# Kernel optimization log

Hardware: AMD Instinct MI355X
Metric: run time of the kernel (lower is better)

The kernel has to match this reference:

```python
import jax, jax.numpy as jnp
import numpy as np

N = 50000
E = 800000
NUM_GRAPHS = 128
X_IN, HID, EDGE_DIM = 64, 64, 16


def setup_inputs() -> dict:
    key = jax.random.key(0)
    ks = jax.random.split(key, 9)
    s = 0.05
    inp = {
        'x': jax.random.normal(ks[0], (N, X_IN), jnp.float32),
        'edge_index': jax.random.randint(ks[1], (2, E), 0, N, dtype=jnp.int32),
        'edge_attr': jax.random.normal(ks[2], (E, EDGE_DIM), jnp.float32),
        'batch': jnp.sort(jax.random.randint(ks[3], (N,), 0, NUM_GRAPHS, dtype=jnp.int32)),
        'w_fc1': jax.random.normal(ks[4], (EDGE_DIM, 1), jnp.float32) * s,
        'b_fc1': jnp.zeros((1,), jnp.float32),
    }
    dims = [(X_IN, HID), (HID, HID * 2), (HID * 2, HID)]
    for i, (din, dout) in enumerate(dims):
        k1, k2, k3 = jax.random.split(ks[5 + i], 3)
        inp[f'w1_{i}'] = jax.random.normal(k1, (din, dout), jnp.float32) * s
        inp[f'b1_{i}'] = jnp.zeros((dout,), jnp.float32)
        inp[f'w2_{i}'] = jax.random.normal(k2, (din, dout), jnp.float32) * s
        inp[f'w3_{i}'] = jax.random.normal(k3, (din, dout), jnp.float32) * s
        inp[f'b3_{i}'] = jnp.zeros((dout,), jnp.float32)
    return inp


def leconv(x, src, dst, ew, w1, b1, w2, w3, b3):
    # PyG LEConv: out_i = lin3(x_i) + sum_{j->i} e_ji * (lin1(x_j) - lin2(x_i))
    a = x @ w1 + b1          # lin1 (bias=True)   [N, out]
    b = x @ w2               # lin2 (bias=False)  [N, out]
    msg = ew[:, None] * (a[src] - b[dst])          # [E, out]
    agg = jax.ops.segment_sum(msg, dst, num_segments=N)
    return agg + x @ w3 + b3  # lin3 (bias=True)


def reference(x, edge_index, edge_attr, batch,
              w_fc1, b_fc1,
              w1_0, b1_0, w2_0, w3_0, b3_0,
              w1_1, b1_1, w2_1, w3_1, b3_1,
              w1_2, b1_2, w2_2, w3_2, b3_2):
    src, dst = edge_index[0], edge_index[1]
    ew = (edge_attr @ w_fc1 + b_fc1)[:, 0]         # fc1(edge_attr).squeeze(-1) -> [E]
    h = jax.nn.elu(leconv(x, src, dst, ew, w1_0, b1_0, w2_0, w3_0, b3_0))
    h = jax.nn.elu(leconv(h, src, dst, ew, w1_1, b1_1, w2_1, w3_1, b3_1))
    h = jax.nn.elu(leconv(h, src, dst, ew, w1_2, b1_2, w2_2, w3_2, b3_2))
    # global max pool over nodes of each graph -> [NUM_GRAPHS, HID]
    return jax.ops.segment_max(h, batch, num_segments=NUM_GRAPHS)
```

## Files before the change

kernel.cpp:

```cpp
#include <hip/hip_runtime.h>
#include <math.h>

#define N_NODES 50000
#define N_EDGES 800000
#define NUM_GRAPHS_ 128
#define SCAN_NB 98
#define NPASS 8
#define NODES_PER_PASS 6250
#define HCHUNKS 128
#define EDGES_PER_CHUNK 6250
#define HWORDS 12500

typedef unsigned short u16;
typedef unsigned int u32;
typedef __attribute__((ext_vector_type(8))) short bf16x8;
typedef __attribute__((ext_vector_type(4))) float f32x4;

__device__ __forceinline__ float elu_f(float v) {
    return v > 0.f ? v : (__expf(v) - 1.f);
}
__device__ __forceinline__ u16 f2bf(float f) {
    u32 u = __float_as_uint(f);
    u += 0x7FFFu + ((u >> 16) & 1u);
    return (u16)(u >> 16);
}
__device__ __forceinline__ float bf2f(u16 h) {
    return __uint_as_float(((u32)h) << 16);
}
__device__ __forceinline__ void bfpair(u32 v, float& lo, float& hi) {
    lo = __uint_as_float(v << 16);
    hi = __uint_as_float(v & 0xFFFF0000u);
}
__device__ __forceinline__ u32 packbf(float lo, float hi) {
    return (u32)f2bf(lo) | ((u32)f2bf(hi) << 16);
}

__global__ void conv_x_kernel(const float* __restrict__ x, u16* __restrict__ xb) {
    int g = blockIdx.x * blockDim.x + threadIdx.x;
    float4 v = ((const float4*)x)[g];
    uint2 o;
    o.x = packbf(v.x, v.y);
    o.y = packbf(v.z, v.w);
    ((uint2*)xb)[g] = o;
}

__global__ void ew_kernel(const float* __restrict__ edge_attr,
                          const float* __restrict__ w_fc1,
                          const float* __restrict__ b_fc1,
                          const int* __restrict__ edge_index,
                          float* __restrict__ ew,
                          u16* __restrict__ dst16) {
    int e = blockIdx.x * blockDim.x + threadIdx.x;
    if (e >= N_EDGES) return;
    const float4* ea = (const float4*)(edge_attr + (size_t)e * 16);
    const float4* wf = (const float4*)w_fc1;
    float acc = b_fc1[0];
#pragma unroll
    for (int i = 0; i < 4; i++) {
        float4 a = ea[i], w = wf[i];
        acc += a.x * w.x + a.y * w.y + a.z * w.z + a.w * w.w;
    }
    ew[e] = acc;
    dst16[e] = (u16)edge_index[N_EDGES + e];
}

__global__ __launch_bounds__(256) void deg_hist_kernel(const u16* __restrict__ dst16,
                                                       u32* __restrict__ partial) {
    __shared__ u32 bins[HWORDS];
    const int c = blockIdx.x >> 1;
    const int p = blockIdx.x & 1;
    const int t = threadIdx.x;
    for (int i = t; i < HWORDS; i += 256) bins[i] = 0;
    __syncthreads();
    const int base = c * EDGES_PER_CHUNK;
    const int nlo = p * 25000;
    for (int i = t; i < EDGES_PER_CHUNK; i += 256) {
        const int b = (int)dst16[base + i] - nlo;
        if ((unsigned)b < 25000u)
            atomicAdd(&bins[b >> 1], 1u << ((b & 1) * 16));
    }
    __syncthreads();
    u32* outp = partial + (size_t)blockIdx.x * HWORDS;
    for (int i = t; i < HWORDS; i += 256) outp[i] = bins[i];
}

__global__ void deg_reduce_kernel(const u32* __restrict__ partial,
                                  u32* __restrict__ deg4) {
    const int tidg = blockIdx.x * 256 + threadIdx.x;
    if (tidg >= 25000) return;
    const int p = (tidg >= HWORDS) ? 1 : 0;
    const int w = tidg - p * HWORDS;
    const int y = blockIdx.y;
    u32 lo = 0, hi = 0;
#pragma unroll 8
    for (int j = 0; j < 32; j++) {
        u32 v = partial[(size_t)(((y * 32 + j) << 1) + p) * HWORDS + w];
        lo += v & 0xFFFFu;
        hi += v >> 16;
    }
    const int n = p * 25000 + 2 * w;
    deg4[(size_t)y * N_NODES + n] = lo;
    deg4[(size_t)y * N_NODES + n + 1] = hi;
}

__global__ __launch_bounds__(256) void scan1_kernel(const u32* __restrict__ deg4,
                                                    int* __restrict__ rowptr,
                                                    int* __restrict__ blk_sums) {
    __shared__ int sh[256];
    const int t = threadIdx.x;
    const int base = blockIdx.x * 512;
    const int i0 = base + 2 * t, i1 = i0 + 1;
    int d0 = 0, d1 = 0;
    if (i0 < N_NODES) {
#pragma unroll
        for (int y = 0; y < 4; y++) {
            d0 += (int)deg4[(size_t)y * N_NODES + i0];
            d1 += (int)deg4[(size_t)y * N_NODES + i1];
        }
    }
    const int pair = d0 + d1;
    int v = pair;
    sh[t] = v;
    __syncthreads();
#pragma unroll
    for (int off = 1; off < 256; off <<= 1) {
        int add = (t >= off) ? sh[t - off] : 0;
        __syncthreads();
        v += add;
        sh[t] = v;
        __syncthreads();
    }
    const int excl = v - pair;
    if (i0 < N_NODES) rowptr[i0] = excl;
    if (i1 < N_NODES) rowptr[i1] = excl + d0;
    if (t == 255) blk_sums[blockIdx.x] = v;
}

__global__ __launch_bounds__(128) void scan2_kernel(const int* __restrict__ blk_sums,
                                                    int* __restrict__ blk_offs,
                                                    int* __restrict__ rowptr) {
    __shared__ int sh[128];
    const int t = threadIdx.x;
    const int orig = (t < SCAN_NB) ? blk_sums[t] : 0;
    int v = orig;
    sh[t] = v;
    __syncthreads();
#pragma unroll
    for (int off = 1; off < 128; off <<= 1) {
        int add = (t >= off) ? sh[t - off] : 0;
        __syncthreads();
        v += add;
        sh[t] = v;
        __syncthreads();
    }
    if (t < SCAN_NB) blk_offs[t] = v - orig;
    if (t == 127) rowptr[N_NODES] = v;
}

__global__ void scan3_kernel(int* __restrict__ rowptr,
                             const int* __restrict__ blk_offs,
                             int* __restrict__ cursor) {
    int i = blockIdx.x * blockDim.x + threadIdx.x;
    if (i >= N_NODES) return;
    int r = rowptr[i] + blk_offs[i >> 9];
    rowptr[i] = r;
    cursor[i] = r;
}

__global__ __launch_bounds__(256) void place_kernel(const int* __restrict__ edge_index,
                                                    const float* __restrict__ ew,
                                                    const u16* __restrict__ dst16,
                                                    int* __restrict__ cursor,
                                                    int2* __restrict__ csr) {
    const int pass = blockIdx.x & (NPASS - 1);
    const int chunk = blockIdx.x >> 3;
    const int lo = pass * NODES_PER_PASS;
    const int hi = lo + NODES_PER_PASS;
    const int base = chunk * 1024 + threadIdx.x;
#pragma unroll
    for (int u = 0; u < 4; u++) {
        const int e = base + u * 256;
        if (e >= N_EDGES) break;
        const int d = (int)dst16[e];
        if (d >= lo && d < hi) {
            int pos = atomicAdd(&cursor[d], 1);
            int2 ent;
            ent.x = edge_index[e];
            ent.y = __float_as_int(ew[e]);
            csr[pos] = ent;
        }
    }
}

template <int DIN, bool WRITE_C>
__global__ __launch_bounds__(256) void gather_kernel(
    const u16* __restrict__ xb, const int* __restrict__ rowptr,
    const int2* __restrict__ csr, u16* __restrict__ sb,
    u16* __restrict__ chb, float* __restrict__ c) {
    constexpr int CG = DIN / 4;
    constexpr int EG = 64 / CG;
    const int gid = blockIdx.x * 256 + threadIdx.x;
    const int node = gid >> 6;
    if (node >= N_NODES) return;
    const int lane = threadIdx.x & 63;
    const int cg = lane & (CG - 1);
    const int eg = lane / CG;
    const int beg = rowptr[node];
    const int end = rowptr[node + 1];
    const uint2* x2 = (const uint2*)xb;

    float a0 = 0.f, a1 = 0.f, a2 = 0.f, a3 = 0.f;
    float b0 = 0.f, b1 = 0.f, b2 = 0.f, b3 = 0.f;
    float wsum = 0.f;

    int p = beg + eg;
    for (; p + EG < end; p += 2 * EG) {
        int2 e0 = csr[p];
        int2 e1 = csr[p + EG];
        float w0 = __int_as_float(e0.y);
        float w1 = __int_as_float(e1.y);
        uint2 v0 = x2[(size_t)e0.x * CG + cg];
        uint2 v1 = x2[(size_t)e1.x * CG + cg];
        float f0, f1, f2, f3, g0, g1, g2, g3;
        bfpair(v0.x, f0, f1); bfpair(v0.y, f2, f3);
        bfpair(v1.x, g0, g1); bfpair(v1.y, g2, g3);
        a0 += w0 * f0; a1 += w0 * f1; a2 += w0 * f2; a3 += w0 * f3;
        b0 += w1 * g0; b1 += w1 * g1; b2 += w1 * g2; b3 += w1 * g3;
        wsum += w0 + w1;
    }
    if (p < end) {
        int2 e0 = csr[p];
        float w0 = __int_as_float(e0.y);
        uint2 v0 = x2[(size_t)e0.x * CG + cg];
        float f0, f1, f2, f3;
        bfpair(v0.x, f0, f1); bfpair(v0.y, f2, f3);
        a0 += w0 * f0; a1 += w0 * f1; a2 += w0 * f2; a3 += w0 * f3;
        wsum += w0;
    }
    a0 += b0; a1 += b1; a2 += b2; a3 += b3;

#pragma unroll
    for (int off = 32; off >= CG; off >>= 1) {
        a0 += __shfl_xor(a0, off);
        a1 += __shfl_xor(a1, off);
        a2 += __shfl_xor(a2, off);
        a3 += __shfl_xor(a3, off);
        wsum += __shfl_xor(wsum, off);
    }

    if (lane < CG) {
        uint2 so;
        so.x = packbf(a0, a1);
        so.y = packbf(a2, a3);
        ((uint2*)sb)[(size_t)node * CG + cg] = so;
        const float cn = WRITE_C ? wsum : c[node];
        uint2 hv = x2[(size_t)node * CG + cg];
        float h0, h1, h2, h3;
        bfpair(hv.x, h0, h1); bfpair(hv.y, h2, h3);
        uint2 co;
        co.x = packbf(cn * h0, cn * h1);
        co.y = packbf(cn * h2, cn * h3);
        ((uint2*)chb)[(size_t)node * CG + cg] = co;
    }
    if (WRITE_C && lane == 0) c[node] = wsum;
}

__global__ void pack_w_kernel(const float* __restrict__ w3_0, const float* __restrict__ w1_0, const float* __restrict__ w2_0,
                              const float* __restrict__ w3_1, const float* __restrict__ w1_1, const float* __restrict__ w2_1,
                              const float* __restrict__ w3_2, const float* __restrict__ w1_2, const float* __restrict__ w2_2,
                              u16* __restrict__ bp0, u16* __restrict__ bp1, u16* __restrict__ bp2) {
    int t = blockIdx.x * blockDim.x + threadIdx.x;
    if (t >= 7680) return;
    int DIN, DOUT, lid;
    const float *w3, *w1, *w2;
    u16* bp;
    if (t < 1536)      { DIN = 64;  DOUT = 64;  lid = t;        w3 = w3_0; w1 = w1_0; w2 = w2_0; bp = bp0; }
    else if (t < 4608) { DIN = 64;  DOUT = 128; lid = t - 1536; w3 = w3_1; w1 = w1_1; w2 = w2_1; bp = bp1; }
    else               { DIN = 128; DOUT = 64;  lid = t - 4608; w3 = w3_2; w1 = w1_2; w2 = w2_2; bp = bp2; }
    const int NT = DOUT / 16;
    const int lane = lid & 63;
    const int fragid = lid >> 6;
    const int chunk = fragid / NT;
    const int ntile = fragid % NT;
    const int n = ntile * 16 + (lane & 15);
    const int kbase = chunk * 32 + (lane >> 4) * 8;
    u16 buf[8];
#pragma unroll
    for (int j = 0; j < 8; j++) {
        int k = kbase + j;
        int region = k / DIN;
        int kk = k - region * DIN;
        float v = (region == 0) ? w3[kk * DOUT + n]
                : (region == 1) ? w1[kk * DOUT + n]
                                : -w2[kk * DOUT + n];
        buf[j] = f2bf(v);
    }
    *(bf16x8*)(bp + ((size_t)lid << 3)) = *(bf16x8*)buf;
}

template <int DIN, int DOUT>
__global__ __launch_bounds__(256) void gemm_mfma(
    const u16* __restrict__ hb, const u16* __restrict__ sb,
    const u16* __restrict__ chb, const u16* __restrict__ Bp,
    const float* __restrict__ cvec, const float* __restrict__ bias1,
    const float* __restrict__ bias3, u16* __restrict__ outp) {
    constexpr int CH = DIN / 32;
    constexpr int CHUNKS = 3 * CH;
    constexpr int NT = DOUT / 16;
    const int tid = threadIdx.x;
    const int wv = tid >> 6;
    const int lane = tid & 63;
    const int l15 = lane & 15;
    const int q = lane >> 4;
    const int mhalf = wv & 1;
    const int nhalf = wv >> 1;
    const int row_base = blockIdx.x * 64 + mhalf * 32;
    const int nt0 = blockIdx.y * 4 + nhalf * 2;

    const int r0 = min(row_base + l15, N_NODES - 1);
    const int r1 = min(row_base + 16 + l15, N_NODES - 1);
    const int qo = q * 8;

    f32x4 acc00 = {0.f, 0.f, 0.f, 0.f};
    f32x4 acc01 = {0.f, 0.f, 0.f, 0.f};
    f32x4 acc10 = {0.f, 0.f, 0.f, 0.f};
    f32x4 acc11 = {0.f, 0.f, 0.f, 0.f};

#pragma unroll
    for (int chunk = 0; chunk < CHUNKS; chunk++) {
        const int region = chunk / CH;
        const int koff = (chunk - region * CH) * 32 + qo;
        const u16* A = (region == 0) ? hb : (region == 1) ? sb : chb;
        bf16x8 a0 = *(const bf16x8*)(A + (size_t)r0 * DIN + koff);
        bf16x8 a1 = *(const bf16x8*)(A + (size_t)r1 * DIN + koff);
        const u16* bp = Bp + (((size_t)(chunk * NT + nt0) * 64 + lane) << 3);
        bf16x8 bf0 = *(const bf16x8*)bp;
        bf16x8 bf1 = *(const bf16x8*)(bp + 64 * 8);
        acc00 = __builtin_amdgcn_mfma_f32_16x16x32_bf16(a0, bf0, acc00, 0, 0, 0);
        acc01 = __builtin_amdgcn_mfma_f32_16x16x32_bf16(a0, bf1, acc01, 0, 0, 0);
        acc10 = __builtin_amdgcn_mfma_f32_16x16x32_bf16(a1, bf0, acc10, 0, 0, 0);
        acc11 = __builtin_amdgcn_mfma_f32_16x16x32_bf16(a1, bf1, acc11, 0, 0, 0);
    }

#pragma unroll
    for (int ni = 0; ni < 2; ni++) {
        const int col = (nt0 + ni) * 16 + l15;
        const float B3 = bias3[col];
        const float B1 = bias1[col];
        const f32x4 am0 = ni ? acc01 : acc00;
        const f32x4 am1 = ni ? acc11 : acc10;
#pragma unroll
        for (int mi = 0; mi < 2; mi++) {
            const f32x4 av = mi ? am1 : am0;
#pragma unroll
            for (int reg = 0; reg < 4; reg++) {
                const int row = row_base + mi * 16 + q * 4 + reg;
                if (row < N_NODES) {
                    const float cv = cvec[row];
                    const float val = av[reg] + B3 + cv * B1;
                    outp[(size_t)row * DOUT + col] = f2bf(elu_f(val));
                }
            }
        }
    }
}

__global__ void pool_kernel(const u16* __restrict__ h,
                            const int* __restrict__ batch,
                            float* __restrict__ out) {
    const int g = blockIdx.x;
    const int tid = threadIdx.x;
    int lo = 0, hi = N_NODES;
    while (lo < hi) { int mid = (lo + hi) >> 1; if (batch[mid] < g) lo = mid + 1; else hi = mid; }
    const int beg = lo;
    lo = beg; hi = N_NODES;
    while (lo < hi) { int mid = (lo + hi) >> 1; if (batch[mid] < g + 1) lo = mid + 1; else hi = mid; }
    const int end = lo;

    __shared__ float red[256];
    const int col = tid & 63;
    const int rg = tid >> 6;
    float m = -3.0e38f;
    for (int r = beg + rg; r < end; r += 4) m = fmaxf(m, bf2f(h[(size_t)r * 64 + col]));
    red[tid] = m;
    __syncthreads();
    if (tid < 64) {
        m = fmaxf(fmaxf(red[tid], red[tid + 64]), fmaxf(red[tid + 128], red[tid + 192]));
        out[g * 64 + tid] = m;
    }
}

extern "C" void kernel_launch(void* const* d_in, const int* in_sizes, int n_in,
                              void* d_out, int out_size, void* d_ws, size_t ws_size,
                              hipStream_t stream) {
    const float* x = (const float*)d_in[0];
    const int* ei = (const int*)d_in[1];
    const float* ea = (const float*)d_in[2];
    const int* batch = (const int*)d_in[3];
    const float* wfc = (const float*)d_in[4];
    const float* bfc = (const float*)d_in[5];
    const float* w1_0 = (const float*)d_in[6];
    const float* b1_0 = (const float*)d_in[7];
    const float* w2_0 = (const float*)d_in[8];
    const float* w3_0 = (const float*)d_in[9];
    const float* b3_0 = (const float*)d_in[10];
    const float* w1_1 = (const float*)d_in[11];
    const float* b1_1 = (const float*)d_in[12];
    const float* w2_1 = (const float*)d_in[13];
    const float* w3_1 = (const float*)d_in[14];
    const float* b3_1 = (const float*)d_in[15];
    const float* w1_2 = (const float*)d_in[16];
    const float* b1_2 = (const float*)d_in[17];
    const float* w2_2 = (const float*)d_in[18];
    const float* w3_2 = (const float*)d_in[19];
    const float* b3_2 = (const float*)d_in[20];
    float* out = (float*)d_out;

    char* ws = (char*)d_ws;
    float* ew      = (float*)(ws);
    float* c       = (float*)(ws + 3200000);
    int*   cursor  = (int*)  (ws + 3600000);
    int*   rowptr  = (int*)  (ws + 3800000);
    int2*  csr     = (int2*) (ws + 4000128);
    u16*   xb      = (u16*)  (ws + 10400128);
    u16*   sb      = (u16*)  (ws + 16800128);
    u16*   chb     = (u16*)  (ws + 29600128);
    u16*   h1      = (u16*)  (ws + 42400128);
    u16*   h2      = (u16*)  (ws + 48800128);
    u16*   h3      = (u16*)  (ws + 61600128);
    u16*   bp0     = (u16*)  (ws + 68000128);
    u16*   bp1     = (u16*)  (ws + 68024704);
    u16*   bp2     = (u16*)  (ws + 68073856);
    int* blk_sums  = (int*)  (ws + 68123008);
    int* blk_offs  = (int*)  (ws + 68123520);
    u16* dst16   = chb;
    u32* deg4    = (u32*)(ws + 31600128);
    u32* partial = (u32*)sb;

    conv_x_kernel<<<3125, 256, 0, stream>>>(x, xb);
    ew_kernel<<<(N_EDGES + 255) / 256, 256, 0, stream>>>(ea, wfc, bfc, ei, ew, dst16);
    pack_w_kernel<<<30, 256, 0, stream>>>(w3_0, w1_0, w2_0, w3_1, w1_1, w2_1,
                                          w3_2, w1_2, w2_2, bp0, bp1, bp2);
    deg_hist_kernel<<<HCHUNKS * 2, 256, 0, stream>>>(dst16, partial);
    deg_reduce_kernel<<<dim3(98, 4), 256, 0, stream>>>(partial, deg4);
    scan1_kernel<<<SCAN_NB, 256, 0, stream>>>(deg4, rowptr, blk_sums);
    scan2_kernel<<<1, 128, 0, stream>>>(blk_sums, blk_offs, rowptr);
    scan3_kernel<<<(N_NODES + 255) / 256, 256, 0, stream>>>(rowptr, blk_offs, cursor);
    place_kernel<<<782 * NPASS, 256, 0, stream>>>(ei, ew, dst16, cursor, csr);

    const int RB = (N_NODES + 63) / 64;
    const int GBLK = (N_NODES * 64 + 255) / 256;

    gather_kernel<64, true><<<GBLK, 256, 0, stream>>>(xb, rowptr, csr, sb, chb, c);
    gemm_mfma<64, 64><<<dim3(RB, 1), 256, 0, stream>>>(xb, sb, chb, bp0, c, b1_0, b3_0, h1);

    gather_kernel<64, false><<<GBLK, 256, 0, stream>>>(h1, rowptr, csr, sb, chb, c);
    gemm_mfma<64, 128><<<dim3(RB, 2), 256, 0, stream>>>(h1, sb, chb, bp1, c, b1_1, b3_1, h2);

    gather_kernel<128, false><<<GBLK, 256, 0, stream>>>(h2, rowptr, csr, sb, chb, c);
    gemm_mfma<128, 64><<<dim3(RB, 1), 256, 0, stream>>>(h2, sb, chb, bp2, c, b1_2, b3_2, h3);

    pool_kernel<<<NUM_GRAPHS_, 256, 0, stream>>>(h3, batch, out);
}
```

Before: 369.8 us.

## Make CSR placement deterministic and reorder last layer to transform-then-gather

```diff
diff --git a/kernel.cpp b/kernel.cpp
--- a/kernel.cpp
+++ b/kernel.cpp
@@ -84,26 +84,24 @@
     for (int i = t; i < HWORDS; i += 256) outp[i] = bins[i];
 }
 
-__global__ void deg_reduce_kernel(const u32* __restrict__ partial,
-                                  u32* __restrict__ deg4) {
-    const int tidg = blockIdx.x * 256 + threadIdx.x;
-    if (tidg >= 25000) return;
-    const int p = (tidg >= HWORDS) ? 1 : 0;
-    const int w = tidg - p * HWORDS;
-    const int y = blockIdx.y;
-    u32 lo = 0, hi = 0;
-#pragma unroll 8
-    for (int j = 0; j < 32; j++) {
-        u32 v = partial[(size_t)(((y * 32 + j) << 1) + p) * HWORDS + w];
-        lo += v & 0xFFFFu;
-        hi += v >> 16;
-    }
-    const int n = p * 25000 + 2 * w;
-    deg4[(size_t)y * N_NODES + n] = lo;
-    deg4[(size_t)y * N_NODES + n + 1] = hi;
-}
-
-__global__ __launch_bounds__(256) void scan1_kernel(const u32* __restrict__ deg4,
+__global__ __launch_bounds__(256) void scan_chunks_kernel(const u32* __restrict__ partial,
+                                                          u32* __restrict__ prefpack,
+                                                          u32* __restrict__ degpack) {
+    const int g = blockIdx.x * 256 + threadIdx.x;
+    if (g >= 25000) return;
+    const int p = (g >= HWORDS) ? 1 : 0;
+    const int wh = g - p * HWORDS;
+    u32 runlo = 0, runhi = 0;
+    for (int c = 0; c < HCHUNKS; c++) {
+        prefpack[(size_t)c * 25000 + g] = runlo | (runhi << 16);
+        u32 v = partial[(size_t)((c << 1) + p) * HWORDS + wh];
+        runlo += v & 0xFFFFu;
+        runhi += v >> 16;
+    }
+    degpack[g] = runlo | (runhi << 16);
+}
+
+__global__ __launch_bounds__(256) void scan1_kernel(const u32* __restrict__ degpack,
                                                     int* __restrict__ rowptr,
                                                     int* __restrict__ blk_sums) {
     __shared__ int sh[256];
@@ -112,11 +110,9 @@
     const int i0 = base + 2 * t, i1 = i0 + 1;
     int d0 = 0, d1 = 0;
     if (i0 < N_NODES) {
-#pragma unroll
-        for (int y = 0; y < 4; y++) {
-            d0 += (int)deg4[(size_t)y * N_NODES + i0];
-            d1 += (int)deg4[(size_t)y * N_NODES + i1];
-        }
+        u32 v = degpack[i0 >> 1];
+        d0 = (int)(v & 0xFFFFu);
+        d1 = (int)(v >> 16);
     }
     const int pair = d0 + d1;
     int v = pair;
@@ -158,36 +154,38 @@
 }
 
 __global__ void scan3_kernel(int* __restrict__ rowptr,
-                             const int* __restrict__ blk_offs,
-                             int* __restrict__ cursor) {
+                             const int* __restrict__ blk_offs) {
     int i = blockIdx.x * blockDim.x + threadIdx.x;
     if (i >= N_NODES) return;
-    int r = rowptr[i] + blk_offs[i >> 9];
-    rowptr[i] = r;
-    cursor[i] = r;
+    rowptr[i] += blk_offs[i >> 9];
 }
 
 __global__ __launch_bounds__(256) void place_kernel(const int* __restrict__ edge_index,
                                                     const float* __restrict__ ew,
                                                     const u16* __restrict__ dst16,
-                                                    int* __restrict__ cursor,
+                                                    const int* __restrict__ rowptr,
+                                                    const u32* __restrict__ prefpack,
                                                     int2* __restrict__ csr) {
+    __shared__ int lcur[NODES_PER_PASS];
     const int pass = blockIdx.x & (NPASS - 1);
-    const int chunk = blockIdx.x >> 3;
+    const int c = blockIdx.x >> 3;
     const int lo = pass * NODES_PER_PASS;
-    const int hi = lo + NODES_PER_PASS;
-    const int base = chunk * 1024 + threadIdx.x;
-#pragma unroll
-    for (int u = 0; u < 4; u++) {
-        const int e = base + u * 256;
-        if (e >= N_EDGES) break;
+    const int t = threadIdx.x;
+    for (int i = t; i < NODES_PER_PASS; i += 256) lcur[i] = 0;
+    __syncthreads();
+    const int base = c * EDGES_PER_CHUNK;
+    for (int i = t; i < EDGES_PER_CHUNK; i += 256) {
+        const int e = base + i;
         const int d = (int)dst16[e];
-        if (d >= lo && d < hi) {
-            int pos = atomicAdd(&cursor[d], 1);
+        const int dl = d - lo;
+        if ((unsigned)dl < (unsigned)NODES_PER_PASS) {
+            u32 pw = prefpack[(size_t)c * 25000 + (d >> 1)];
+            int pref = (int)((pw >> ((d & 1) * 16)) & 0xFFFFu);
+            int lpos = atomicAdd(&lcur[dl], 1);
             int2 ent;
             ent.x = edge_index[e];
             ent.y = __float_as_int(ew[e]);
-            csr[pos] = ent;
+            csr[rowptr[d] + pref + lpos] = ent;
         }
     }
 }
@@ -271,31 +269,50 @@
                               u16* __restrict__ bp0, u16* __restrict__ bp1, u16* __restrict__ bp2) {
     int t = blockIdx.x * blockDim.x + threadIdx.x;
     if (t >= 7680) return;
-    int DIN, DOUT, lid;
-    const float *w3, *w1, *w2;
-    u16* bp;
-    if (t < 1536)      { DIN = 64;  DOUT = 64;  lid = t;        w3 = w3_0; w1 = w1_0; w2 = w2_0; bp = bp0; }
-    else if (t < 4608) { DIN = 64;  DOUT = 128; lid = t - 1536; w3 = w3_1; w1 = w1_1; w2 = w2_1; bp = bp1; }
-    else               { DIN = 128; DOUT = 64;  lid = t - 4608; w3 = w3_2; w1 = w1_2; w2 = w2_2; bp = bp2; }
-    const int NT = DOUT / 16;
-    const int lane = lid & 63;
-    const int fragid = lid >> 6;
-    const int chunk = fragid / NT;
-    const int ntile = fragid % NT;
-    const int n = ntile * 16 + (lane & 15);
-    const int kbase = chunk * 32 + (lane >> 4) * 8;
     u16 buf[8];
-#pragma unroll
-    for (int j = 0; j < 8; j++) {
-        int k = kbase + j;
-        int region = k / DIN;
-        int kk = k - region * DIN;
-        float v = (region == 0) ? w3[kk * DOUT + n]
-                : (region == 1) ? w1[kk * DOUT + n]
-                                : -w2[kk * DOUT + n];
-        buf[j] = f2bf(v);
-    }
-    *(bf16x8*)(bp + ((size_t)lid << 3)) = *(bf16x8*)buf;
+    if (t < 4608) {
+        int DIN, DOUT, lid;
+        const float *w3, *w1, *w2;
+        u16* bp;
+        if (t < 1536) { DIN = 64; DOUT = 64;  lid = t;        w3 = w3_0; w1 = w1_0; w2 = w2_0; bp = bp0; }
+        else          { DIN = 64; DOUT = 128; lid = t - 1536; w3 = w3_1; w1 = w1_1; w2 = w2_1; bp = bp1; }
+        const int NT = DOUT / 16;
+        const int lane = lid & 63;
+        const int fragid = lid >> 6;
+        const int chunk = fragid / NT;
+        const int ntile = fragid % NT;
+        const int n = ntile * 16 + (lane & 15);
+        const int kbase = chunk * 32 + (lane >> 4) * 8;
+#pragma unroll
+        for (int j = 0; j < 8; j++) {
+            int k = kbase + j;
+            int region = k / DIN;
+            int kk = k - region * DIN;
+            float v = (region == 0) ? w3[kk * DOUT + n]
+                    : (region == 1) ? w1[kk * DOUT + n]
+                                    : -w2[kk * DOUT + n];
+            buf[j] = f2bf(v);
+        }
+        *(bf16x8*)(bp + ((size_t)lid << 3)) = *(bf16x8*)buf;
+    } else {
+        const int lid = t - 4608;
+        const int NT = 12;
+        const int lane = lid & 63;
+        const int fragid = lid >> 6;
+        const int chunk = fragid / NT;
+        const int ntile = fragid % NT;
+        const int n = ntile * 16 + (lane & 15);
+        const int kbase = chunk * 32 + (lane >> 4) * 8;
+#pragma unroll
+        for (int j = 0; j < 8; j++) {
+            int k = kbase + j;
+            float v = (n < 64)  ? w3_2[k * 64 + n]
+                    : (n < 128) ? -w2_2[k * 64 + (n - 64)]
+                                : w1_2[k * 64 + (n - 128)];
+            buf[j] = f2bf(v);
+        }
+        *(bf16x8*)(bp2 + ((size_t)lid << 3)) = *(bf16x8*)buf;
+    }
 }
 
 template <int DIN, int DOUT>
@@ -362,6 +379,130 @@
                 }
             }
         }
+    }
+}
+
+__global__ __launch_bounds__(256) void gemm_wide_kernel(
+    const u16* __restrict__ hb, const u16* __restrict__ Bp,
+    u16* __restrict__ zuy) {
+    constexpr int NT = 12;
+    const int tid = threadIdx.x;
+    const int wv = tid >> 6;
+    const int lane = tid & 63;
+    const int l15 = lane & 15;
+    const int q = lane >> 4;
+    const int row_base = blockIdx.x * 64 + (wv & 1) * 32;
+    const int nt0 = blockIdx.y * 4 + (wv >> 1) * 2;
+
+    const int r0 = min(row_base + l15, N_NODES - 1);
+    const int r1 = min(row_base + 16 + l15, N_NODES - 1);
+    const int qo = q * 8;
+
+    f32x4 acc00 = {0.f, 0.f, 0.f, 0.f};
+    f32x4 acc01 = {0.f, 0.f, 0.f, 0.f};
+    f32x4 acc10 = {0.f, 0.f, 0.f, 0.f};
+    f32x4 acc11 = {0.f, 0.f, 0.f, 0.f};
+
+#pragma unroll
+    for (int chunk = 0; chunk < 4; chunk++) {
+        const int koff = chunk * 32 + qo;
+        bf16x8 a0 = *(const bf16x8*)(hb + (size_t)r0 * 128 + koff);
+        bf16x8 a1 = *(const bf16x8*)(hb + (size_t)r1 * 128 + koff);
+        const u16* bp = Bp + (((size_t)(chunk * NT + nt0) * 64 + lane) << 3);
+        bf16x8 bf0 = *(const bf16x8*)bp;
+        bf16x8 bf1 = *(const bf16x8*)(bp + 64 * 8);
+        acc00 = __builtin_amdgcn_mfma_f32_16x16x32_bf16(a0, bf0, acc00, 0, 0, 0);
+        acc01 = __builtin_amdgcn_mfma_f32_16x16x32_bf16(a0, bf1, acc01, 0, 0, 0);
+        acc10 = __builtin_amdgcn_mfma_f32_16x16x32_bf16(a1, bf0, acc10, 0, 0, 0);
+        acc11 = __builtin_amdgcn_mfma_f32_16x16x32_bf16(a1, bf1, acc11, 0, 0, 0);
+    }
+
+#pragma unroll
+    for (int ni = 0; ni < 2; ni++) {
+        const int col = (nt0 + ni) * 16 + l15;
+        const f32x4 am0 = ni ? acc01 : acc00;
+        const f32x4 am1 = ni ? acc11 : acc10;
+#pragma unroll
+        for (int mi = 0; mi < 2; mi++) {
+            const f32x4 av = mi ? am1 : am0;
+#pragma unroll
+            for (int reg = 0; reg < 4; reg++) {
+                const int row = row_base + mi * 16 + q * 4 + reg;
+                if (row < N_NODES)
+                    zuy[(size_t)row * 192 + col] = f2bf(av[reg]);
+            }
+        }
+    }
+}
+
+__global__ __launch_bounds__(256) void gather2_kernel(
+    const u16* __restrict__ zuy, const int* __restrict__ rowptr,
+    const int2* __restrict__ csr, const float* __restrict__ c,
+    const float* __restrict__ bias1, const float* __restrict__ bias3,
+    u16* __restrict__ h3) {
+    constexpr int CG = 16, EG = 4;
+    const int gid = blockIdx.x * 256 + threadIdx.x;
+    const int node = gid >> 6;
+    if (node >= N_NODES) return;
+    const int lane = threadIdx.x & 63;
+    const int cg = lane & (CG - 1);
+    const int eg = lane >> 4;
+    const int beg = rowptr[node];
+    const int end = rowptr[node + 1];
+
+    float a0 = 0.f, a1 = 0.f, a2 = 0.f, a3 = 0.f;
+    float b0 = 0.f, b1 = 0.f, b2 = 0.f, b3 = 0.f;
+
+    int p = beg + eg;
+    for (; p + EG < end; p += 2 * EG) {
+        int2 e0 = csr[p];
+        int2 e1 = csr[p + EG];
+        float w0 = __int_as_float(e0.y);
+        float w1 = __int_as_float(e1.y);
+        uint2 v0 = ((const uint2*)(zuy + (size_t)e0.x * 192 + 128))[cg];
+        uint2 v1 = ((const uint2*)(zuy + (size_t)e1.x * 192 + 128))[cg];
+        float f0, f1, f2, f3, g0, g1, g2, g3;
+        bfpair(v0.x, f0, f1); bfpair(v0.y, f2, f3);
+        bfpair(v1.x, g0, g1); bfpair(v1.y, g2, g3);
+        a0 += w0 * f0; a1 += w0 * f1; a2 += w0 * f2; a3 += w0 * f3;
+        b0 += w1 * g0; b1 += w1 * g1; b2 += w1 * g2; b3 += w1 * g3;
+    }
+    if (p < end) {
+        int2 e0 = csr[p];
+        float w0 = __int_as_float(e0.y);
+        uint2 v0 = ((const uint2*)(zuy + (size_t)e0.x * 192 + 128))[cg];
+        float f0, f1, f2, f3;
+        bfpair(v0.x, f0, f1); bfpair(v0.y, f2, f3);
+        a0 += w0 * f0; a1 += w0 * f1; a2 += w0 * f2; a3 += w0 * f3;
+    }
+    a0 += b0; a1 += b1; a2 += b2; a3 += b3;
+
+#pragma unroll
+    for (int off = 32; off >= CG; off >>= 1) {
+        a0 += __shfl_xor(a0, off);
+        a1 += __shfl_xor(a1, off);
+        a2 += __shfl_xor(a2, off);
+        a3 += __shfl_xor(a3, off);
+    }
+
+    if (lane < CG) {
+        const float cn = c[node];
+        const u16* zr = zuy + (size_t)node * 192;
+        uint2 zv = ((const uint2*)zr)[cg];
+        uint2 uv = ((const uint2*)(zr + 64))[cg];
+        float z0, z1, z2, z3, u0, u1, u2, u3;
+        bfpair(zv.x, z0, z1); bfpair(zv.y, z2, z3);
+        bfpair(uv.x, u0, u1); bfpair(uv.y, u2, u3);
+        const float4 b3v = *(const float4*)(bias3 + cg * 4);
+        const float4 b1v = *(const float4*)(bias1 + cg * 4);
+        float o0 = elu_f(z0 + cn * u0 + a0 + b3v.x + cn * b1v.x);
+        float o1 = elu_f(z1 + cn * u1 + a1 + b3v.y + cn * b1v.y);
+        float o2 = elu_f(z2 + cn * u2 + a2 + b3v.z + cn * b1v.z);
+        float o3 = elu_f(z3 + cn * u3 + a3 + b3v.w + cn * b1v.w);
+        uint2 o;
+        o.x = packbf(o0, o1);
+        o.y = packbf(o2, o3);
+        ((uint2*)h3)[(size_t)node * CG + cg] = o;
     }
 }
 
@@ -419,7 +560,6 @@
     char* ws = (char*)d_ws;
     float* ew      = (float*)(ws);
     float* c       = (float*)(ws + 3200000);
-    int*   cursor  = (int*)  (ws + 3600000);
     int*   rowptr  = (int*)  (ws + 3800000);
     int2*  csr     = (int2*) (ws + 4000128);
     u16*   xb      = (u16*)  (ws + 10400128);
@@ -434,19 +574,21 @@
     int* blk_sums  = (int*)  (ws + 68123008);
     int* blk_offs  = (int*)  (ws + 68123520);
     u16* dst16   = chb;
-    u32* deg4    = (u32*)(ws + 31600128);
+    u32* degpack = (u32*)(ws + 31600128);
     u32* partial = (u32*)sb;
+    u32* prefpack = (u32*)h2;
+    u16* zuy     = sb;
 
     conv_x_kernel<<<3125, 256, 0, stream>>>(x, xb);
     ew_kernel<<<(N_EDGES + 255) / 256, 256, 0, stream>>>(ea, wfc, bfc, ei, ew, dst16);
     pack_w_kernel<<<30, 256, 0, stream>>>(w3_0, w1_0, w2_0, w3_1, w1_1, w2_1,
                                           w3_2, w1_2, w2_2, bp0, bp1, bp2);
     deg_hist_kernel<<<HCHUNKS * 2, 256, 0, stream>>>(dst16, partial);
-    deg_reduce_kernel<<<dim3(98, 4), 256, 0, stream>>>(partial, deg4);
-    scan1_kernel<<<SCAN_NB, 256, 0, stream>>>(deg4, rowptr, blk_sums);
+    scan_chunks_kernel<<<98, 256, 0, stream>>>(partial, prefpack, degpack);
+    scan1_kernel<<<SCAN_NB, 256, 0, stream>>>(degpack, rowptr, blk_sums);
     scan2_kernel<<<1, 128, 0, stream>>>(blk_sums, blk_offs, rowptr);
-    scan3_kernel<<<(N_NODES + 255) / 256, 256, 0, stream>>>(rowptr, blk_offs, cursor);
-    place_kernel<<<782 * NPASS, 256, 0, stream>>>(ei, ew, dst16, cursor, csr);
+    scan3_kernel<<<(N_NODES + 255) / 256, 256, 0, stream>>>(rowptr, blk_offs);
+    place_kernel<<<HCHUNKS * NPASS, 256, 0, stream>>>(ei, ew, dst16, rowptr, prefpack, csr);
 
     const int RB = (N_NODES + 63) / 64;
     const int GBLK = (N_NODES * 64 + 255) / 256;
@@ -457,8 +599,8 @@
     gather_kernel<64, false><<<GBLK, 256, 0, stream>>>(h1, rowptr, csr, sb, chb, c);
     gemm_mfma<64, 128><<<dim3(RB, 2), 256, 0, stream>>>(h1, sb, chb, bp1, c, b1_1, b3_1, h2);
 
-    gather_kernel<128, false><<<GBLK, 256, 0, stream>>>(h2, rowptr, csr, sb, chb, c);
-    gemm_mfma<128, 64><<<dim3(RB, 1), 256, 0, stream>>>(h2, sb, chb, bp2, c, b1_2, b3_2, h3);
+    gemm_wide_kernel<<<dim3(RB, 3), 256, 0, stream>>>(h2, bp2, zuy);
+    gather2_kernel<<<GBLK, 256, 0, stream>>>(zuy, rowptr, csr, c, b1_2, b3_2, h3);
 
     pool_kernel<<<NUM_GRAPHS_, 256, 0, stream>>>(h3, batch, out);
 }
```

Result: faster. 349.7 us (-5.4%).
